# Kernel tuning notes

Measured on AMD Instinct MI355X. Metric: run time of the kernel, lower is better.

The kernel has to match this reference:

```python
import jax, jax.numpy as jnp
import numpy as np

B, O, T, D, H, DOUT = 32, 4096, 16384, 128, 128, 128
EPS = 1e-3  # keras BatchNormalization default epsilon


def setup_inputs() -> dict:
    key = jax.random.key(0)
    ks = jax.random.split(key, 8)
    std = 0.05  # keras RandomNormal default stddev
    return {
        "obj_vecs": jax.random.normal(ks[0], (B, O, D), jnp.float32),
        "pred_vecs": jax.random.normal(ks[1], (B, T, D), jnp.float32),
        "edges": jax.random.randint(ks[2], (B, T, 2), 0, O, dtype=jnp.int32),
        # net1: [3D -> H] -> BN -> ReLU -> [H -> 2H+Dout] -> BN -> ReLU
        "W1": jax.random.normal(ks[3], (3 * D, H), jnp.float32) * std,
        "b1": jnp.zeros((H,), jnp.float32),
        "g1": jnp.ones((H,), jnp.float32),
        "be1": jnp.zeros((H,), jnp.float32),
        "W2": jax.random.normal(ks[4], (H, 2 * H + DOUT), jnp.float32) * std,
        "b2": jnp.zeros((2 * H + DOUT,), jnp.float32),
        "g2": jnp.ones((2 * H + DOUT,), jnp.float32),
        "be2": jnp.zeros((2 * H + DOUT,), jnp.float32),
        # net2: [H -> H] -> BN -> ReLU -> [H -> Dout] -> BN -> ReLU
        "W3": jax.random.normal(ks[5], (H, H), jnp.float32) * std,
        "b3": jnp.zeros((H,), jnp.float32),
        "g3": jnp.ones((H,), jnp.float32),
        "be3": jnp.zeros((H,), jnp.float32),
        "W4": jax.random.normal(ks[6], (H, DOUT), jnp.float32) * std,
        "b4": jnp.zeros((DOUT,), jnp.float32),
        "g4": jnp.ones((DOUT,), jnp.float32),
        "be4": jnp.zeros((DOUT,), jnp.float32),
    }


def _block(x, W, b, g, be):
    # Dense -> BatchNorm(inference: mean=0, var=1) -> ReLU
    h = x @ W + b
    h = h * (g / jnp.sqrt(1.0 + EPS)) + be
    return jax.nn.relu(h)


def reference(obj_vecs, pred_vecs, edges,
              W1, b1, g1, be1, W2, b2, g2, be2,
              W3, b3, g3, be3, W4, b4, g4, be4):
    s_idx = edges[..., 0]  # (B, T)
    o_idx = edges[..., 1]  # (B, T)

    # gather subject / object vectors: (B, T, D)
    cur_s = jnp.take_along_axis(obj_vecs, s_idx[..., None], axis=1)
    cur_o = jnp.take_along_axis(obj_vecs, o_idx[..., None], axis=1)
    cur_t = jnp.concatenate([cur_s, pred_vecs, cur_o], axis=2)  # (B, T, 3D)

    new_t = _block(_block(cur_t, W1, b1, g1, be1), W2, b2, g2, be2)  # (B, T, 2H+Dout)
    new_s = new_t[..., :H]
    new_p = new_t[..., H:H + DOUT]
    new_o = new_t[..., H + DOUT:]

    # NOTE: original TF code overwrites the s-scatter with the o-scatter,
    # so only object-side messages contribute. scatter_nd sums duplicates.
    bidx = jnp.arange(B)[:, None]  # (B, 1), broadcasts over T
    pooled = jnp.zeros((B, O, H), new_t.dtype).at[bidx, o_idx].add(new_o)
    counts = jnp.zeros((B, O), new_t.dtype).at[bidx, o_idx].add(1.0)
    pooled = pooled / jnp.clip(counts, 1.0, None)[..., None]  # avg pooling

    new_obj = _block(_block(pooled, W3, b3, g3, be3), W4, b4, g4, be4)  # (B, O, Dout)
    return new_obj, new_p
```

## Files before the change

kernel.cpp:

```cpp
#include <hip/hip_runtime.h>
#include <hip/hip_bf16.h>
#include <stdint.h>

#define Bn 32
#define On 4096
#define Tn 16384
#define Dn 128

typedef short short8 __attribute__((ext_vector_type(8)));
typedef float f32x4 __attribute__((ext_vector_type(4)));

__device__ inline short f2bf(float f) {
  union { float f; uint32_t u; } v; v.f = f;
  uint32_t u = v.u;
  uint32_t r = u + 0x7fffu + ((u >> 16) & 1u);
  return (short)(r >> 16);
}
__device__ inline float bf2f(unsigned short u) {
  union { uint32_t ui; float f; } cv; cv.ui = ((uint32_t)u) << 16; return cv.f;
}
__device__ inline uint32_t pack2bf(float a, float b) {
  return ((uint32_t)(uint16_t)f2bf(a)) | (((uint32_t)(uint16_t)f2bf(b)) << 16);
}
__device__ inline float bflo(uint32_t u) { union { uint32_t i; float f; } c; c.i = u << 16; return c.f; }
__device__ inline float bfhi(uint32_t u) { union { uint32_t i; float f; } c; c.i = u & 0xffff0000u; return c.f; }

__global__ void prep_weights(const float* __restrict__ W1, const float* __restrict__ W2,
                             const float* __restrict__ W3, const float* __restrict__ W4,
                             const float* __restrict__ b1, const float* __restrict__ g1, const float* __restrict__ be1,
                             const float* __restrict__ b2, const float* __restrict__ g2, const float* __restrict__ be2,
                             const float* __restrict__ b3, const float* __restrict__ g3, const float* __restrict__ be3,
                             const float* __restrict__ b4, const float* __restrict__ g4, const float* __restrict__ be4,
                             short* __restrict__ w1t, short* __restrict__ w2t,
                             short* __restrict__ w3t, short* __restrict__ w4t,
                             float* __restrict__ add1g, float* __restrict__ add2g,
                             float* __restrict__ add3g, float* __restrict__ add4g) {
  const float invs = 1.0f / sqrtf(1.001f);
  int i = blockIdx.x * 256 + threadIdx.x;
  if (i < 49152) {
    int n = i / 384, k = i % 384;
    w1t[i] = f2bf(W1[k * 128 + n] * g1[n] * invs);
  } else if (i < 81920) {
    int j = i - 49152;
    int n = j / 128, k = j % 128;
    int c2 = 128 + n;
    w2t[j] = f2bf(W2[k * 384 + c2] * g2[c2] * invs);
  } else if (i < 98304) {
    int j = i - 81920;
    int n = j / 128, k = j % 128;
    w3t[j] = f2bf(W3[k * 128 + n] * g3[n] * invs);
  } else if (i < 114688) {
    int j = i - 98304;
    int n = j / 128, k = j % 128;
    w4t[j] = f2bf(W4[k * 128 + n] * g4[n] * invs);
  } else if (i < 114816) {
    int n = i - 114688;
    add1g[n] = b1[n] * g1[n] * invs + be1[n];
  } else if (i < 115072) {
    int n = i - 114816;
    int c2 = 128 + n;
    add2g[n] = b2[c2] * g2[c2] * invs + be2[c2];
  } else if (i < 115200) {
    int n = i - 115072;
    add3g[n] = b3[n] * g3[n] * invs + be3[n];
  } else if (i < 115328) {
    int n = i - 115200;
    add4g[n] = b4[n] * g4[n] * invs + be4[n];
  }
}

__global__ __launch_bounds__(1024) void sort_kernel(
    const int* __restrict__ edges, int* __restrict__ hist_g,
    int* __restrict__ offs_g, unsigned short* __restrict__ eidx)
{
  __shared__ int h[4096];
  __shared__ int of[4096];
  __shared__ int sd[1024];
  int b = blockIdx.x, tid = threadIdx.x;
#pragma unroll
  for (int i = 0; i < 4; i++) h[tid + i * 1024] = 0;
  __syncthreads();
  int ov[16];
#pragma unroll
  for (int j = 0; j < 16; j++) {
    int t = j * 1024 + tid;
    ov[j] = edges[((size_t)(b * Tn + t)) * 2 + 1];
    atomicAdd(&h[ov[j]], 1);
  }
  __syncthreads();
  int base = tid * 4;
  int hh[4]; int s = 0;
#pragma unroll
  for (int j = 0; j < 4; j++) { hh[j] = h[base + j]; s += hh[j]; }
  sd[tid] = s;
  int tsum = s;
  for (int off = 1; off < 1024; off <<= 1) {
    __syncthreads();
    int t = (tid >= off) ? sd[tid - off] : 0;
    __syncthreads();
    sd[tid] += t;
  }
  __syncthreads();
  int excl = sd[tid] - tsum + b * Tn;
#pragma unroll
  for (int j = 0; j < 4; j++) {
    of[base + j] = excl;
    offs_g[b * On + base + j] = excl;
    hist_g[b * On + base + j] = hh[j];
    excl += hh[j];
  }
  __syncthreads();
#pragma unroll
  for (int i = 0; i < 4; i++) h[tid + i * 1024] = 0;
  __syncthreads();
#pragma unroll
  for (int j = 0; j < 16; j++) {
    int t = j * 1024 + tid;
    int pos = of[ov[j]] + atomicAdd(&h[ov[j]], 1);
    eidx[pos] = (unsigned short)t;
  }
}

__global__ __launch_bounds__(512, 2) void objproj(
    const float* __restrict__ obj, const short* __restrict__ w1t,
    const float* __restrict__ add1g, unsigned short* __restrict__ objSO)
{
  __shared__ __align__(16) char lds[81920];
  const int WOF = 0, AOF = 65536;
  int tid = threadIdx.x;
  {
    int n = tid >> 2, q = tid & 3;
    int swz = (n & 7) << 4;
    const short* s1 = w1t + n * 384 + q * 32;
    const short* s2 = w1t + n * 384 + 256 + q * 32;
#pragma unroll
    for (int i = 0; i < 4; i++) {
      *(short8*)(lds + WOF + n * 256 + ((q * 64 + i * 16) ^ swz)) = *(const short8*)(s1 + i * 8);
      *(short8*)(lds + WOF + 32768 + n * 256 + ((q * 64 + i * 16) ^ swz)) = *(const short8*)(s2 + i * 8);
    }
  }
  int wave = tid >> 6, lane = tid & 63;
  int l15 = lane & 15, l4 = lane >> 4;
  int mg = wave >> 2, ng = wave & 3;
  int r = tid >> 3, seg = tid & 7;
  int rswz = (r & 7) << 4;

  for (int it = 0; it < 4; it++) {
    int row0 = (blockIdx.x * 4 + it) * 64;
    if (it) __syncthreads();
    {
      const float* src = obj + (size_t)(row0 + r) * Dn + seg * 16;
      float4 v0 = *(const float4*)(src);
      float4 v1 = *(const float4*)(src + 4);
      float4 v2 = *(const float4*)(src + 8);
      float4 v3 = *(const float4*)(src + 12);
      short8 p0, p1;
      p0[0]=f2bf(v0.x); p0[1]=f2bf(v0.y); p0[2]=f2bf(v0.z); p0[3]=f2bf(v0.w);
      p0[4]=f2bf(v1.x); p0[5]=f2bf(v1.y); p0[6]=f2bf(v1.z); p0[7]=f2bf(v1.w);
      p1[0]=f2bf(v2.x); p1[1]=f2bf(v2.y); p1[2]=f2bf(v2.z); p1[3]=f2bf(v2.w);
      p1[4]=f2bf(v3.x); p1[5]=f2bf(v3.y); p1[6]=f2bf(v3.z); p1[7]=f2bf(v3.w);
      *(short8*)(lds + AOF + r * 256 + ((seg * 32) ^ rswz)) = p0;
      *(short8*)(lds + AOF + r * 256 + ((seg * 32 + 16) ^ rswz)) = p1;
    }
    __syncthreads();
#pragma unroll
    for (int half = 0; half < 2; half++) {
      f32x4 acc[2][2] = {};
#pragma unroll
      for (int kk = 0; kk < 4; kk++) {
        short8 a[2], bb[2];
#pragma unroll
        for (int m = 0; m < 2; m++) {
          int row = mg * 32 + m * 16 + l15;
          a[m] = *(short8*)(lds + AOF + row * 256 + ((kk * 64 + 16 * l4) ^ ((row & 7) << 4)));
        }
#pragma unroll
        for (int n = 0; n < 2; n++) {
          int nr = ng * 32 + n * 16 + l15;
          bb[n] = *(short8*)(lds + WOF + half * 32768 + nr * 256 + ((kk * 64 + 16 * l4) ^ ((nr & 7) << 4)));
        }
#pragma unroll
        for (int m = 0; m < 2; m++)
#pragma unroll
          for (int n = 0; n < 2; n++)
            acc[m][n] = __builtin_amdgcn_mfma_f32_16x16x32_bf16(a[m], bb[n], acc[m][n], 0, 0, 0);
      }
#pragma unroll
      for (int n = 0; n < 2; n++) {
        int col = ng * 32 + n * 16 + l15;
        float addv = half ? 0.0f : add1g[col];
#pragma unroll
        for (int m = 0; m < 2; m++)
#pragma unroll
          for (int rr = 0; rr < 4; rr++) {
            int row = mg * 32 + m * 16 + l4 * 4 + rr;
            objSO[(size_t)(row0 + row) * 256 + half * 128 + col] =
                (unsigned short)f2bf(acc[m][n][rr] + addv);
          }
      }
    }
  }
}

__global__ __launch_bounds__(512, 2) void edge_mlp(
    const float* __restrict__ pred, const int* __restrict__ edges,
    const unsigned short* __restrict__ objSO,
    const short* __restrict__ w1t, const short* __restrict__ w2t,
    const float* __restrict__ add2g,
    float* __restrict__ out_p, unsigned short* __restrict__ o_scr)
{
  __shared__ __align__(16) char lds[132096];
  const int W1P = 0;
  const int W2O = 32768;
  const int ADD2 = 98304;
  const int H1B = 99328;

  int tid = threadIdx.x;
  {
    int n = tid >> 2, q = tid & 3;
    int swz = (n & 7) << 4;
    const short* src = w1t + n * 384 + 128 + q * 32;
#pragma unroll
    for (int i = 0; i < 4; i++)
      *(short8*)(lds + W1P + n * 256 + ((q * 64 + i * 16) ^ swz)) = *(const short8*)(src + i * 8);
  }
  {
    int n = tid >> 1, q = tid & 1;
    int swz = (n & 7) << 4;
    const short* src = w2t + n * 128 + q * 64;
#pragma unroll
    for (int i = 0; i < 8; i++)
      *(short8*)(lds + W2O + n * 256 + ((q * 128 + i * 16) ^ swz)) = *(const short8*)(src + i * 8);
  }
  if (tid < 256) *(float*)(lds + ADD2 + tid * 4) = add2g[tid];
  __syncthreads();

  int wave = tid >> 6, lane = tid & 63;
  int l15 = lane & 15, l4 = lane >> 4;
  char* h1w = lds + H1B + wave * 4096;
  int hswz = (l15 & 7) << 4;

  size_t wrow0 = ((size_t)blockIdx.x * 8 + wave) * 256;
  int b_ = (int)(wrow0 >> 14);
  const char* soBase = (const char*)objSO + (size_t)b_ * On * 512;

  float4 pp[8];
  uint2 gsv[8], gov[8];
  int2 e;

  auto load_ep = [&](int j) {
    size_t gr = wrow0 + (size_t)j * 16 + l15;
    e = *(const int2*)&edges[gr * 2];
    const float* pr = pred + gr * 128 + l4 * 8;
#pragma unroll
    for (int kk = 0; kk < 4; kk++) {
      pp[2 * kk]     = *(const float4*)(pr + kk * 32);
      pp[2 * kk + 1] = *(const float4*)(pr + kk * 32 + 4);
    }
  };
  auto load_g = [&]() {
    const char* bs = soBase + (size_t)e.x * 512 + l4 * 8;
    const char* bo = soBase + (size_t)e.y * 512 + 256 + l4 * 8;
#pragma unroll
    for (int n = 0; n < 8; n++) {
      gsv[n] = *(const uint2*)(bs + n * 32);
      gov[n] = *(const uint2*)(bo + n * 32);
    }
  };

  load_ep(0);
  load_g();

  for (int j = 0; j < 16; ++j) {
    size_t gr = wrow0 + (size_t)j * 16 + l15;

    short8 af[4];
#pragma unroll
    for (int kk = 0; kk < 4; kk++) {
      float4 a0 = pp[2 * kk], a1 = pp[2 * kk + 1];
      short8 a;
      a[0]=f2bf(a0.x); a[1]=f2bf(a0.y); a[2]=f2bf(a0.z); a[3]=f2bf(a0.w);
      a[4]=f2bf(a1.x); a[5]=f2bf(a1.y); a[6]=f2bf(a1.z); a[7]=f2bf(a1.w);
      af[kk] = a;
    }
    if (j + 1 < 16) load_ep(j + 1);

    f32x4 acc1[8] = {};
    __builtin_amdgcn_s_setprio(1);
#pragma unroll
    for (int kk = 0; kk < 4; kk++) {
#pragma unroll
      for (int n = 0; n < 8; n++) {
        short8 wf = *(short8*)(lds + W1P + (n * 16 + l15) * 256 + ((kk * 64 + 16 * l4) ^ hswz));
        acc1[n] = __builtin_amdgcn_mfma_f32_16x16x32_bf16(wf, af[kk], acc1[n], 0, 0, 0);
      }
    }
    __builtin_amdgcn_s_setprio(0);

#pragma unroll
    for (int n = 0; n < 8; n++) {
      float v0 = fmaxf(acc1[n][0] + bflo(gsv[n].x) + bflo(gov[n].x), 0.0f);
      float v1 = fmaxf(acc1[n][1] + bfhi(gsv[n].x) + bfhi(gov[n].x), 0.0f);
      float v2 = fmaxf(acc1[n][2] + bflo(gsv[n].y) + bflo(gov[n].y), 0.0f);
      float v3 = fmaxf(acc1[n][3] + bfhi(gsv[n].y) + bfhi(gov[n].y), 0.0f);
      uint2 hd; hd.x = pack2bf(v0, v1); hd.y = pack2bf(v2, v3);
      *(uint2*)(h1w + l15 * 256 + ((n * 32 + l4 * 8) ^ hswz)) = hd;
    }
    if (j + 1 < 16) load_g();

    short8 af2[4];
#pragma unroll
    for (int kk = 0; kk < 4; kk++)
      af2[kk] = *(short8*)(h1w + l15 * 256 + ((kk * 64 + 16 * l4) ^ hswz));

#pragma unroll
    for (int half = 0; half < 2; half++) {
      f32x4 acc2[8] = {};
      __builtin_amdgcn_s_setprio(1);
#pragma unroll
      for (int kk = 0; kk < 4; kk++) {
#pragma unroll
        for (int n = 0; n < 8; n++) {
          short8 wf = *(short8*)(lds + W2O + (half * 128 + n * 16 + l15) * 256 + ((kk * 64 + 16 * l4) ^ hswz));
          acc2[n] = __builtin_amdgcn_mfma_f32_16x16x32_bf16(wf, af2[kk], acc2[n], 0, 0, 0);
        }
      }
      __builtin_amdgcn_s_setprio(0);
      if (half == 0) {
#pragma unroll
        for (int n = 0; n < 8; n++) {
          float4 ad = *(float4*)(lds + ADD2 + (n * 16 + l4 * 4) * 4);
          float4 ov;
          ov.x = fmaxf(acc2[n][0] + ad.x, 0.0f);
          ov.y = fmaxf(acc2[n][1] + ad.y, 0.0f);
          ov.z = fmaxf(acc2[n][2] + ad.z, 0.0f);
          ov.w = fmaxf(acc2[n][3] + ad.w, 0.0f);
          *(float4*)(out_p + gr * 128 + n * 16 + l4 * 4) = ov;
        }
      } else {
#pragma unroll
        for (int n = 0; n < 8; n++) {
          float4 ad = *(float4*)(lds + ADD2 + 512 + (n * 16 + l4 * 4) * 4);
          float v0 = fmaxf(acc2[n][0] + ad.x, 0.0f);
          float v1 = fmaxf(acc2[n][1] + ad.y, 0.0f);
          float v2 = fmaxf(acc2[n][2] + ad.z, 0.0f);
          float v3 = fmaxf(acc2[n][3] + ad.w, 0.0f);
          uint2 od; od.x = pack2bf(v0, v1); od.y = pack2bf(v2, v3);
          *(uint2*)((char*)o_scr + gr * 256 + (n * 16 + l4 * 4) * 2) = od;
        }
      }
    }
  }
}

__global__ __launch_bounds__(256) void obj_mlp(
    const unsigned short* __restrict__ o_scr, const int* __restrict__ hist,
    const int* __restrict__ offs, const unsigned short* __restrict__ eidx,
    float* __restrict__ out_obj,
    const short* __restrict__ w3t, const short* __restrict__ w4t,
    const float* __restrict__ add3g, const float* __restrict__ add4g)
{
  __shared__ short xs[64][136];
  __shared__ short hs[64][136];
  int row0 = blockIdx.x * 64;
  int tid = threadIdx.x;

  {
    int r = tid >> 2, seg = tid & 3;
    int rg = row0 + r;
    int bb_ = rg >> 12;
    int cnt = hist[rg], start = offs[rg];
    float sum[32];
#pragma unroll
    for (int j = 0; j < 32; j++) sum[j] = 0.f;
    for (int k = 0; k < cnt; k++) {
      int t = eidx[start + k];
      const unsigned short* src = o_scr + ((size_t)(bb_ * Tn + t)) * 128 + seg * 32;
#pragma unroll
      for (int i = 0; i < 4; i++) {
        short8 v = *(const short8*)(src + i * 8);
#pragma unroll
        for (int j = 0; j < 8; j++) sum[i * 8 + j] += bf2f((unsigned short)v[j]);
      }
    }
    float ic = 1.0f / fmaxf((float)cnt, 1.0f);
#pragma unroll
    for (int i = 0; i < 4; i++) {
      short8 pk;
#pragma unroll
      for (int j = 0; j < 8; j++) pk[j] = f2bf(sum[i * 8 + j] * ic);
      *(short8*)&xs[r][seg * 32 + i * 8] = pk;
    }
  }
  __syncthreads();

  int wave = tid >> 6, lane = tid & 63;
  int l15 = lane & 15, l4 = lane >> 4;
  int n0 = wave * 32;

  short8 w3r[2][4], w4r[2][4];
#pragma unroll
  for (int n = 0; n < 2; n++)
#pragma unroll
    for (int kk = 0; kk < 4; kk++) {
      w3r[n][kk] = *(const short8*)&w3t[(n0 + n * 16 + l15) * 128 + kk * 32 + 8 * l4];
      w4r[n][kk] = *(const short8*)&w4t[(n0 + n * 16 + l15) * 128 + kk * 32 + 8 * l4];
    }

  f32x4 acc[4][2] = {};
#pragma unroll
  for (int kk = 0; kk < 4; kk++) {
    int k0 = kk * 32;
    short8 a[4];
#pragma unroll
    for (int m = 0; m < 4; m++) a[m] = *(short8*)&xs[m * 16 + l15][k0 + 8 * l4];
#pragma unroll
    for (int m = 0; m < 4; m++)
#pragma unroll
      for (int n = 0; n < 2; n++)
        acc[m][n] = __builtin_amdgcn_mfma_f32_16x16x32_bf16(a[m], w3r[n][kk], acc[m][n], 0, 0, 0);
  }
#pragma unroll
  for (int n = 0; n < 2; n++) {
    int col = n0 + n * 16 + l15;
    float ad = add3g[col];
#pragma unroll
    for (int m = 0; m < 4; m++)
#pragma unroll
      for (int rr = 0; rr < 4; rr++) {
        float v = fmaxf(acc[m][n][rr] + ad, 0.0f);
        hs[m * 16 + l4 * 4 + rr][col] = f2bf(v);
      }
  }
  __syncthreads();

  f32x4 acc2[4][2] = {};
#pragma unroll
  for (int kk = 0; kk < 4; kk++) {
    int k0 = kk * 32;
    short8 a[4];
#pragma unroll
    for (int m = 0; m < 4; m++) a[m] = *(short8*)&hs[m * 16 + l15][k0 + 8 * l4];
#pragma unroll
    for (int m = 0; m < 4; m++)
#pragma unroll
      for (int n = 0; n < 2; n++)
        acc2[m][n] = __builtin_amdgcn_mfma_f32_16x16x32_bf16(a[m], w4r[n][kk], acc2[m][n], 0, 0, 0);
  }
#pragma unroll
  for (int n = 0; n < 2; n++) {
    int col = n0 + n * 16 + l15;
    float ad = add4g[col];
#pragma unroll
    for (int m = 0; m < 4; m++)
#pragma unroll
      for (int rr = 0; rr < 4; rr++) {
        int row = m * 16 + l4 * 4 + rr;
        float v = fmaxf(acc2[m][n][rr] + ad, 0.0f);
        out_obj[(size_t)(row0 + row) * 128 + col] = v;
      }
  }
}

extern "C" void kernel_launch(void* const* d_in, const int* in_sizes, int n_in,
                              void* d_out, int out_size, void* d_ws, size_t ws_size,
                              hipStream_t stream) {
  const float* obj  = (const float*)d_in[0];
  const float* pred = (const float*)d_in[1];
  const int*   edges= (const int*)d_in[2];
  const float* W1 = (const float*)d_in[3];
  const float* b1 = (const float*)d_in[4];
  const float* g1 = (const float*)d_in[5];
  const float* be1= (const float*)d_in[6];
  const float* W2 = (const float*)d_in[7];
  const float* b2 = (const float*)d_in[8];
  const float* g2 = (const float*)d_in[9];
  const float* be2= (const float*)d_in[10];
  const float* W3 = (const float*)d_in[11];
  const float* b3 = (const float*)d_in[12];
  const float* g3 = (const float*)d_in[13];
  const float* be3= (const float*)d_in[14];
  const float* W4 = (const float*)d_in[15];
  const float* b4 = (const float*)d_in[16];
  const float* g4 = (const float*)d_in[17];
  const float* be4= (const float*)d_in[18];

  float* out_obj = (float*)d_out;
  float* out_p   = (float*)d_out + (size_t)Bn * On * 128;
  unsigned short* objSO = (unsigned short*)d_out;

  char* ws = (char*)d_ws;
  short* w1t = (short*)(ws);
  short* w2t = (short*)(ws + 49152 * 2);
  short* w3t = (short*)(ws + (49152 + 32768) * 2);
  short* w4t = (short*)(ws + (49152 + 32768 + 16384) * 2);
  float* add1g = (float*)(ws + 229376);
  float* add2g = (float*)(ws + 229888);
  float* add3g = (float*)(ws + 230912);
  float* add4g = (float*)(ws + 231424);

  const size_t OFF_HIST = 262144;
  const size_t OFF_OFFS = OFF_HIST + 524288;
  const size_t OFF_EIDX = OFF_OFFS + 1048576;
  const size_t OFF_OSCR = 4194304;

  int* hist = (int*)(ws + OFF_HIST);
  int* offs = (int*)(ws + OFF_OFFS);
  unsigned short* eidx = (unsigned short*)(ws + OFF_EIDX);
  unsigned short* o_scr = (unsigned short*)(ws + OFF_OSCR);

  prep_weights<<<451, 256, 0, stream>>>(W1, W2, W3, W4,
      b1, g1, be1, b2, g2, be2, b3, g3, be3, b4, g4, be4,
      w1t, w2t, w3t, w4t, add1g, add2g, add3g, add4g);
  sort_kernel<<<Bn, 1024, 0, stream>>>(edges, hist, offs, eidx);
  objproj<<<512, 512, 0, stream>>>(obj, w1t, add1g, objSO);
  edge_mlp<<<256, 512, 0, stream>>>(pred, edges, objSO, w1t, w2t, add2g,
      out_p, o_scr);
  obj_mlp<<<(Bn * On) / 64, 256, 0, stream>>>(o_scr, hist, offs, eidx, out_obj,
      w3t, w4t, add3g, add4g);
}
```

Baseline: 327.3 us.

## Merge weight prep into sort kernel and keep edge MLP hidden in registers

Weight preprocessing now runs in extra blocks of the sort kernel, which removes one kernel launch. In the edge MLP, the first layer's output stays in registers and feeds the second GEMM directly through 16x16x16 bf16 MFMAs, so the per-wave LDS round trip for the hidden tile goes away. Blocks grow to 1024 threads with 16 waves of 128 rows each, and the smaller LDS footprint allows this. The cost is twice as many MFMA instructions in the second GEMM, more register pressure, and one block per CU.

```diff
diff --git a/kernel.cpp b/kernel.cpp
--- a/kernel.cpp
+++ b/kernel.cpp
@@ -8,6 +8,7 @@
 #define Dn 128
 
 typedef short short8 __attribute__((ext_vector_type(8)));
+typedef short short4v __attribute__((ext_vector_type(4)));
 typedef float f32x4 __attribute__((ext_vector_type(4)));
 
 __device__ inline short f2bf(float f) {
@@ -25,54 +26,55 @@
 __device__ inline float bflo(uint32_t u) { union { uint32_t i; float f; } c; c.i = u << 16; return c.f; }
 __device__ inline float bfhi(uint32_t u) { union { uint32_t i; float f; } c; c.i = u & 0xffff0000u; return c.f; }
 
-__global__ void prep_weights(const float* __restrict__ W1, const float* __restrict__ W2,
-                             const float* __restrict__ W3, const float* __restrict__ W4,
-                             const float* __restrict__ b1, const float* __restrict__ g1, const float* __restrict__ be1,
-                             const float* __restrict__ b2, const float* __restrict__ g2, const float* __restrict__ be2,
-                             const float* __restrict__ b3, const float* __restrict__ g3, const float* __restrict__ be3,
-                             const float* __restrict__ b4, const float* __restrict__ g4, const float* __restrict__ be4,
-                             short* __restrict__ w1t, short* __restrict__ w2t,
-                             short* __restrict__ w3t, short* __restrict__ w4t,
-                             float* __restrict__ add1g, float* __restrict__ add2g,
-                             float* __restrict__ add3g, float* __restrict__ add4g) {
-  const float invs = 1.0f / sqrtf(1.001f);
-  int i = blockIdx.x * 256 + threadIdx.x;
-  if (i < 49152) {
-    int n = i / 384, k = i % 384;
-    w1t[i] = f2bf(W1[k * 128 + n] * g1[n] * invs);
-  } else if (i < 81920) {
-    int j = i - 49152;
-    int n = j / 128, k = j % 128;
-    int c2 = 128 + n;
-    w2t[j] = f2bf(W2[k * 384 + c2] * g2[c2] * invs);
-  } else if (i < 98304) {
-    int j = i - 81920;
-    int n = j / 128, k = j % 128;
-    w3t[j] = f2bf(W3[k * 128 + n] * g3[n] * invs);
-  } else if (i < 114688) {
-    int j = i - 98304;
-    int n = j / 128, k = j % 128;
-    w4t[j] = f2bf(W4[k * 128 + n] * g4[n] * invs);
-  } else if (i < 114816) {
-    int n = i - 114688;
-    add1g[n] = b1[n] * g1[n] * invs + be1[n];
-  } else if (i < 115072) {
-    int n = i - 114816;
-    int c2 = 128 + n;
-    add2g[n] = b2[c2] * g2[c2] * invs + be2[c2];
-  } else if (i < 115200) {
-    int n = i - 115072;
-    add3g[n] = b3[n] * g3[n] * invs + be3[n];
-  } else if (i < 115328) {
-    int n = i - 115200;
-    add4g[n] = b4[n] * g4[n] * invs + be4[n];
-  }
-}
-
-__global__ __launch_bounds__(1024) void sort_kernel(
+__global__ __launch_bounds__(1024) void prep_sort(
     const int* __restrict__ edges, int* __restrict__ hist_g,
-    int* __restrict__ offs_g, unsigned short* __restrict__ eidx)
+    int* __restrict__ offs_g, unsigned short* __restrict__ eidx,
+    const float* __restrict__ W1, const float* __restrict__ W2,
+    const float* __restrict__ W3, const float* __restrict__ W4,
+    const float* __restrict__ b1, const float* __restrict__ g1, const float* __restrict__ be1,
+    const float* __restrict__ b2, const float* __restrict__ g2, const float* __restrict__ be2,
+    const float* __restrict__ b3, const float* __restrict__ g3, const float* __restrict__ be3,
+    const float* __restrict__ b4, const float* __restrict__ g4, const float* __restrict__ be4,
+    short* __restrict__ w1t, short* __restrict__ w2t,
+    short* __restrict__ w3t, short* __restrict__ w4t,
+    float* __restrict__ add1g, float* __restrict__ add2g,
+    float* __restrict__ add3g, float* __restrict__ add4g)
 {
+  if (blockIdx.x >= 32) {
+    const float invs = 1.0f / sqrtf(1.001f);
+    int i = (blockIdx.x - 32) * 1024 + threadIdx.x;
+    if (i < 49152) {
+      int n = i / 384, k = i % 384;
+      w1t[i] = f2bf(W1[k * 128 + n] * g1[n] * invs);
+    } else if (i < 81920) {
+      int j = i - 49152;
+      int n = j / 128, k = j % 128;
+      int c2 = 128 + n;
+      w2t[j] = f2bf(W2[k * 384 + c2] * g2[c2] * invs);
+    } else if (i < 98304) {
+      int j = i - 81920;
+      int n = j / 128, k = j % 128;
+      w3t[j] = f2bf(W3[k * 128 + n] * g3[n] * invs);
+    } else if (i < 114688) {
+      int j = i - 98304;
+      int n = j / 128, k = j % 128;
+      w4t[j] = f2bf(W4[k * 128 + n] * g4[n] * invs);
+    } else if (i < 114816) {
+      int n = i - 114688;
+      add1g[n] = b1[n] * g1[n] * invs + be1[n];
+    } else if (i < 115072) {
+      int n = i - 114816;
+      int c2 = 128 + n;
+      add2g[n] = b2[c2] * g2[c2] * invs + be2[c2];
+    } else if (i < 115200) {
+      int n = i - 115072;
+      add3g[n] = b3[n] * g3[n] * invs + be3[n];
+    } else if (i < 115328) {
+      int n = i - 115200;
+      add4g[n] = b4[n] * g4[n] * invs + be4[n];
+    }
+    return;
+  }
   __shared__ int h[4096];
   __shared__ int of[4096];
   __shared__ int sd[1024];
@@ -202,45 +204,44 @@
   }
 }
 
-__global__ __launch_bounds__(512, 2) void edge_mlp(
+__global__ __launch_bounds__(1024, 1) void edge_mlp(
     const float* __restrict__ pred, const int* __restrict__ edges,
     const unsigned short* __restrict__ objSO,
     const short* __restrict__ w1t, const short* __restrict__ w2t,
     const float* __restrict__ add2g,
     float* __restrict__ out_p, unsigned short* __restrict__ o_scr)
 {
-  __shared__ __align__(16) char lds[132096];
+  __shared__ __align__(16) char lds[99328];
   const int W1P = 0;
   const int W2O = 32768;
   const int ADD2 = 98304;
-  const int H1B = 99328;
 
   int tid = threadIdx.x;
+  {
+    int n = tid >> 3, q = tid & 7;
+    int swz = (n & 7) << 4;
+    const short* src = w1t + n * 384 + 128 + q * 16;
+    short8 v0 = *(const short8*)(src);
+    short8 v1 = *(const short8*)(src + 8);
+    *(short8*)(lds + W1P + n * 256 + ((q * 32) ^ swz)) = v0;
+    *(short8*)(lds + W1P + n * 256 + ((q * 32 + 16) ^ swz)) = v1;
+  }
   {
     int n = tid >> 2, q = tid & 3;
     int swz = (n & 7) << 4;
-    const short* src = w1t + n * 384 + 128 + q * 32;
+    const short* src = w2t + n * 128 + q * 32;
 #pragma unroll
     for (int i = 0; i < 4; i++)
-      *(short8*)(lds + W1P + n * 256 + ((q * 64 + i * 16) ^ swz)) = *(const short8*)(src + i * 8);
-  }
-  {
-    int n = tid >> 1, q = tid & 1;
-    int swz = (n & 7) << 4;
-    const short* src = w2t + n * 128 + q * 64;
-#pragma unroll
-    for (int i = 0; i < 8; i++)
-      *(short8*)(lds + W2O + n * 256 + ((q * 128 + i * 16) ^ swz)) = *(const short8*)(src + i * 8);
+      *(short8*)(lds + W2O + n * 256 + ((q * 64 + i * 16) ^ swz)) = *(const short8*)(src + i * 8);
   }
   if (tid < 256) *(float*)(lds + ADD2 + tid * 4) = add2g[tid];
   __syncthreads();
 
   int wave = tid >> 6, lane = tid & 63;
   int l15 = lane & 15, l4 = lane >> 4;
-  char* h1w = lds + H1B + wave * 4096;
   int hswz = (l15 & 7) << 4;
 
-  size_t wrow0 = ((size_t)blockIdx.x * 8 + wave) * 256;
+  size_t wrow0 = ((size_t)blockIdx.x * 16 + wave) * 128;
   int b_ = (int)(wrow0 >> 14);
   const char* soBase = (const char*)objSO + (size_t)b_ * On * 512;
 
@@ -271,7 +272,7 @@
   load_ep(0);
   load_g();
 
-  for (int j = 0; j < 16; ++j) {
+  for (int j = 0; j < 8; ++j) {
     size_t gr = wrow0 + (size_t)j * 16 + l15;
 
     short8 af[4];
@@ -283,7 +284,7 @@
       a[4]=f2bf(a1.x); a[5]=f2bf(a1.y); a[6]=f2bf(a1.z); a[7]=f2bf(a1.w);
       af[kk] = a;
     }
-    if (j + 1 < 16) load_ep(j + 1);
+    if (j + 1 < 8) load_ep(j + 1);
 
     f32x4 acc1[8] = {};
     __builtin_amdgcn_s_setprio(1);
@@ -297,57 +298,43 @@
     }
     __builtin_amdgcn_s_setprio(0);
 
+    short4v hb[8];
 #pragma unroll
     for (int n = 0; n < 8; n++) {
       float v0 = fmaxf(acc1[n][0] + bflo(gsv[n].x) + bflo(gov[n].x), 0.0f);
       float v1 = fmaxf(acc1[n][1] + bfhi(gsv[n].x) + bfhi(gov[n].x), 0.0f);
       float v2 = fmaxf(acc1[n][2] + bflo(gsv[n].y) + bflo(gov[n].y), 0.0f);
       float v3 = fmaxf(acc1[n][3] + bfhi(gsv[n].y) + bfhi(gov[n].y), 0.0f);
-      uint2 hd; hd.x = pack2bf(v0, v1); hd.y = pack2bf(v2, v3);
-      *(uint2*)(h1w + l15 * 256 + ((n * 32 + l4 * 8) ^ hswz)) = hd;
-    }
-    if (j + 1 < 16) load_g();
-
-    short8 af2[4];
-#pragma unroll
-    for (int kk = 0; kk < 4; kk++)
-      af2[kk] = *(short8*)(h1w + l15 * 256 + ((kk * 64 + 16 * l4) ^ hswz));
-
-#pragma unroll
-    for (int half = 0; half < 2; half++) {
-      f32x4 acc2[8] = {};
+      union { uint32_t u[2]; short4v v; } cv;
+      cv.u[0] = pack2bf(v0, v1);
+      cv.u[1] = pack2bf(v2, v3);
+      hb[n] = cv.v;
+    }
+    if (j + 1 < 8) load_g();
+
+#pragma unroll
+    for (int cg = 0; cg < 16; cg++) {
+      f32x4 acc2 = {};
+      const char* wbase = lds + W2O + (size_t)(cg * 16 + l15) * 256;
       __builtin_amdgcn_s_setprio(1);
 #pragma unroll
-      for (int kk = 0; kk < 4; kk++) {
-#pragma unroll
-        for (int n = 0; n < 8; n++) {
-          short8 wf = *(short8*)(lds + W2O + (half * 128 + n * 16 + l15) * 256 + ((kk * 64 + 16 * l4) ^ hswz));
-          acc2[n] = __builtin_amdgcn_mfma_f32_16x16x32_bf16(wf, af2[kk], acc2[n], 0, 0, 0);
-        }
+      for (int n = 0; n < 8; n++) {
+        short4v wf = *(const short4v*)(wbase + ((n * 32 + l4 * 8) ^ hswz));
+        acc2 = __builtin_amdgcn_mfma_f32_16x16x16bf16_1k(wf, hb[n], acc2, 0, 0, 0);
       }
       __builtin_amdgcn_s_setprio(0);
-      if (half == 0) {
-#pragma unroll
-        for (int n = 0; n < 8; n++) {
-          float4 ad = *(float4*)(lds + ADD2 + (n * 16 + l4 * 4) * 4);
-          float4 ov;
-          ov.x = fmaxf(acc2[n][0] + ad.x, 0.0f);
-          ov.y = fmaxf(acc2[n][1] + ad.y, 0.0f);
-          ov.z = fmaxf(acc2[n][2] + ad.z, 0.0f);
-          ov.w = fmaxf(acc2[n][3] + ad.w, 0.0f);
-          *(float4*)(out_p + gr * 128 + n * 16 + l4 * 4) = ov;
-        }
+      int colp = cg * 16 + l4 * 4;
+      float4 ad = *(float4*)(lds + ADD2 + colp * 4);
+      float v0 = fmaxf(acc2[0] + ad.x, 0.0f);
+      float v1 = fmaxf(acc2[1] + ad.y, 0.0f);
+      float v2 = fmaxf(acc2[2] + ad.z, 0.0f);
+      float v3 = fmaxf(acc2[3] + ad.w, 0.0f);
+      if (cg < 8) {
+        float4 ov; ov.x = v0; ov.y = v1; ov.z = v2; ov.w = v3;
+        *(float4*)(out_p + gr * 128 + colp) = ov;
       } else {
-#pragma unroll
-        for (int n = 0; n < 8; n++) {
-          float4 ad = *(float4*)(lds + ADD2 + 512 + (n * 16 + l4 * 4) * 4);
-          float v0 = fmaxf(acc2[n][0] + ad.x, 0.0f);
-          float v1 = fmaxf(acc2[n][1] + ad.y, 0.0f);
-          float v2 = fmaxf(acc2[n][2] + ad.z, 0.0f);
-          float v3 = fmaxf(acc2[n][3] + ad.w, 0.0f);
-          uint2 od; od.x = pack2bf(v0, v1); od.y = pack2bf(v2, v3);
-          *(uint2*)((char*)o_scr + gr * 256 + (n * 16 + l4 * 4) * 2) = od;
-        }
+        uint2 od; od.x = pack2bf(v0, v1); od.y = pack2bf(v2, v3);
+        *(uint2*)((char*)o_scr + gr * 256 + (colp - 128) * 2) = od;
       }
     }
   }
@@ -509,12 +496,11 @@
   unsigned short* eidx = (unsigned short*)(ws + OFF_EIDX);
   unsigned short* o_scr = (unsigned short*)(ws + OFF_OSCR);
 
-  prep_weights<<<451, 256, 0, stream>>>(W1, W2, W3, W4,
-      b1, g1, be1, b2, g2, be2, b3, g3, be3, b4, g4, be4,
+  prep_sort<<<145, 1024, 0, stream>>>(edges, hist, offs, eidx,
+      W1, W2, W3, W4, b1, g1, be1, b2, g2, be2, b3, g3, be3, b4, g4, be4,
       w1t, w2t, w3t, w4t, add1g, add2g, add3g, add4g);
-  sort_kernel<<<Bn, 1024, 0, stream>>>(edges, hist, offs, eidx);
   objproj<<<512, 512, 0, stream>>>(obj, w1t, add1g, objSO);
-  edge_mlp<<<256, 512, 0, stream>>>(pred, edges, objSO, w1t, w2t, add2g,
+  edge_mlp<<<256, 1024, 0, stream>>>(pred, edges, objSO, w1t, w2t, add2g,
       out_p, o_scr);
   obj_mlp<<<(Bn * On) / 64, 256, 0, stream>>>(o_scr, hist, offs, eidx, out_obj,
       w3t, w4t, add3g, add4g);
```

Result: slower. 879.1 us (+168.6%).
